# Kernel tuning notes

Measured on AMD Instinct MI355X. Metric: run time of the kernel, lower is better.

## Reference

```python
import jax, jax.numpy as jnp
import numpy as np

HBV_LO = jnp.array([1.0, 50.0, 0.05, 0.01, 0.001, 0.2, 0.0, 0.0, -2.5, 0.5, 0.0, 0.0, 0.3, 0.0], dtype=jnp.float32)
HBV_HI = jnp.array([6.0, 1000.0, 0.9, 0.5, 0.2, 1.0, 10.0, 100.0, 2.5, 10.0, 0.1, 0.2, 5.0, 1.0], dtype=jnp.float32)
TDLST = (1, 13)  # 1-based indices of dynamic parameters (BETA, BETAET)
PRECS = 1e-5


def setup_inputs() -> dict:
    key = jax.random.key(0)
    k1, k2 = jax.random.split(key)
    Nstep, Ngrid, mu = 365, 1000, 16
    x = jax.random.uniform(k1, (Nstep, Ngrid, 3), dtype=jnp.float32)  # [P, T, ETpot]
    parameters = jax.random.uniform(k2, (Nstep, Ngrid, 14, mu), dtype=jnp.float32)
    return {"x": x, "parameters": parameters, "staind": Nstep - 1}


def _hbv_run(x, parameters, staind):
    mu = parameters.shape[-1]
    Nstep, Ngrid, _ = x.shape
    # scale raw [0,1] params to physical ranges: [Nstep, Ngrid, 14, mu]
    parAllTrans = HBV_LO[None, None, :, None] + parameters * (HBV_HI - HBV_LO)[None, None, :, None]
    # dynamic params (tdlst) vary per timestep; others frozen at timestep staind
    dynmask = jnp.zeros((14,), jnp.float32).at[jnp.array([ix - 1 for ix in TDLST])].set(1.0)
    m = dynmask[None, None, :, None]
    parFull = parAllTrans * m + parAllTrans[staind][None] * (1.0 - m)

    s0 = jnp.full((Ngrid, mu), 0.001, dtype=jnp.float32)
    init = (s0, s0, s0, s0, s0)  # SNOWPACK, MELTWATER, SM, SUZ, SLZ

    def step(state, xs):
        SP, MW, SM, SUZ, SLZ = state
        Pv, Tv, Ev, par = xs
        P = Pv[:, None]
        T = Tv[:, None]
        ETp = Ev[:, None]
        BETA, FC, K0, K1, K2, LP, PERCp, UZL, TT, CFMAX, CFR, CWH, BETAET, C = [par[:, i, :] for i in range(14)]
        RAIN = P * (T >= TT).astype(jnp.float32)
        SNOW = P * (T < TT).astype(jnp.float32)
        SP = SP + SNOW
        melt = jnp.minimum(jnp.maximum(CFMAX * (T - TT), 0.0), SP)
        MW = MW + melt
        SP = SP - melt
        refr = jnp.minimum(jnp.maximum(CFR * CFMAX * (TT - T), 0.0), MW)
        SP = SP + refr
        MW = MW - refr
        tosoil = jnp.maximum(MW - CWH * SP, 0.0)
        MW = MW - tosoil
        wet = jnp.clip((SM / FC) ** BETA, 0.0, 1.0)
        recharge = (RAIN + tosoil) * wet
        excess = jnp.maximum(SM - FC, 0.0)
        SM = SM - excess
        evapf = jnp.clip((SM / (LP * FC)) ** BETAET, 0.0, 1.0)
        ETact = jnp.minimum(SM, ETp * evapf)
        SM = jnp.maximum(SM - ETact, PRECS)
        SM = SM + RAIN + tosoil - recharge
        cap = jnp.minimum(SLZ, C * SLZ * (1.0 - jnp.minimum(SM / FC, 1.0)))
        SM = jnp.maximum(SM + cap, PRECS)
        SLZ = jnp.maximum(SLZ - cap, PRECS)
        SUZ = SUZ + recharge + excess
        PERC = jnp.minimum(SUZ, PERCp)
        SUZ = SUZ - PERC
        Q0 = K0 * jnp.maximum(SUZ - UZL, 0.0)
        SUZ = SUZ - Q0
        Q1 = K1 * SUZ
        SUZ = SUZ - Q1
        SLZ = SLZ + PERC
        Q2 = K2 * SLZ
        SLZ = SLZ - Q2
        return (SP, MW, SM, SUZ, SLZ), Q0 + Q1 + Q2

    xs = (x[:, :, 0], x[:, :, 1], x[:, :, 2], parFull)
    _, Qsimmu = jax.lax.scan(step, init, xs)  # [Nstep, Ngrid, mu]
    return Qsimmu.mean(-1)[:, :, None]  # muwts=None, routOpt=False -> [Nstep, Ngrid, 1]


def reference(x, parameters, staind):
    return _hbv_run(x, parameters, staind)
```

## Files before the change

### kernel.cpp

```cpp
#include <hip/hip_runtime.h>


static constexpr int   NSTEP = 365;
static constexpr int   NGRID = 1000;
static constexpr int   MU    = 16;
static constexpr float PRECS = 1e-5f;
static constexpr int   QPAD  = 68;

__global__ __launch_bounds__(64)
__attribute__((amdgpu_waves_per_eu(1, 1)))
void hbv_kernel(const float* __restrict__ x,
                const float* __restrict__ par,
                const int*   __restrict__ staind_p,
                float*       __restrict__ out)
{
    __shared__ float qlds[NSTEP * QPAD];

    const int lane = threadIdx.x;
    const int m    = lane & 15;
    const int gl   = lane >> 4;
    const int gbase = blockIdx.x * 4;
    const int g    = gbase + gl;
    const int staind = *staind_p;

    const size_t tstride = (size_t)NGRID * 14 * MU;
    const int    xstride = NGRID * 3;
    const int    lp = g * (14 * MU) + m;
    const int    lx = g * 3;

    const float* ps = par + (size_t)staind * tstride + lp;
    const float FC    = 50.0f  + ps[ 1*MU] * (1000.0f - 50.0f);
    const float K0    = 0.05f  + ps[ 2*MU] * (0.9f  - 0.05f);
    const float K1    = 0.01f  + ps[ 3*MU] * (0.5f  - 0.01f);
    const float K2    = 0.001f + ps[ 4*MU] * (0.2f  - 0.001f);
    const float LP    = 0.2f   + ps[ 5*MU] * (1.0f  - 0.2f);
    const float PERCp =          ps[ 6*MU] * 10.0f;
    const float UZL   =          ps[ 7*MU] * 100.0f;
    const float TT    = -2.5f  + ps[ 8*MU] * 5.0f;
    const float CFMAX = 0.5f   + ps[ 9*MU] * (10.0f - 0.5f);
    const float CRF   =          ps[10*MU] * 0.1f * CFMAX;
    const float CWH   =          ps[11*MU] * 0.2f;
    const float C     =          ps[13*MU] * 1.0f;
    const float rFC   = 1.0f / FC;
    const float lgFC   = __builtin_amdgcn_logf(FC);
    const float dlg    = lgFC - __builtin_amdgcn_logf(LP * FC);
    const float K1c    = 1.0f - K1;
    const float K2c    = 1.0f - K2;
    const float nK0UZL = -K0 * UZL;

    float SP = 1e-3f, MW = 1e-3f, SM = 1e-3f, SUZ = 1e-3f, SLZ = 1e-3f;

    auto step = [&](float P, float T, float E, float p0, float p12) -> float {
        const float BETA    = fmaf(p0, 5.0f, 1.0f);
        const float BETAET  = fmaf(p12, 4.7f, 0.3f);
        const float dT      = T - TT;
        const float acap    = CFMAX * dT;
        const float bcap    = CRF * (-dT);
        const bool  rc      = (T >= TT);
        const float RAIN    = rc ? P : 0.0f;
        const float SNOW    = rc ? 0.0f : P;
        const float smsuz   = SUZ + SM;

        const float SP1  = SP + SNOW;
        const float melt = __builtin_amdgcn_fmed3f(acap, 0.0f, SP1);
        const float SP2  = SP1 - melt;
        const float MW1  = MW + melt;
        const float refr = __builtin_amdgcn_fmed3f(bcap, 0.0f, MW1);
        const float MW2  = MW1 - refr;
        const float SP3  = SP2 + refr;
        const float lim  = CWH * SP3;
        const float tosoil = fmaxf(MW2 - lim, 0.0f);
        SP = SP3;
        MW = fminf(MW2, lim);

        const float SM1    = fminf(SM, FC);
        const float SUZe   = smsuz - SM1;
        const float lg     = __builtin_amdgcn_logf(SM);
        const float uc     = fminf(lg - lgFC, 0.0f);
        const float wet    = __builtin_amdgcn_exp2f(BETA * uc);
        const float evapf  = __builtin_amdgcn_exp2f(BETAET * fminf(uc + dlg, 0.0f));
        const float SM2    = fmaxf(fmaf(-E, evapf, SM1), PRECS);
        const float rt     = RAIN + tosoil;
        const float recharge = rt * wet;
        const float SM3    = (SM2 + rt) - recharge;
        const float capf   = fmaxf(fmaf(-SM3, rFC, 1.0f), 0.0f);
        const float cap    = (C * SLZ) * capf;
        SM = fmaxf(SM3 + cap, PRECS);
        const float SLZ1   = fmaxf(SLZ - cap, PRECS);

        const float SUZ1 = SUZe + recharge;
        const float PERC = fminf(SUZ1, PERCp);
        const float SUZ2 = fmaxf(SUZ1 - PERCp, 0.0f);
        const float Q0   = fmaxf(fmaf(K0, SUZ2, nK0UZL), 0.0f);
        const float SUZ3 = SUZ2 - Q0;
        const float Q1   = K1 * SUZ3;
        SUZ = K1c * SUZ3;
        const float SLZ2 = SLZ1 + PERC;
        const float Q2   = K2 * SLZ2;
        SLZ = K2c * SLZ2;

        return Q0 + Q1 + Q2;
    };

    float aP[10], aT[10], aE[10], a0[10], a12[10];
    float cP[10], cT[10], cE[10], c0[10], c12[10];
    const float* prow = par;
    const float* xrow = x;

#define LOADB(BP, BT, BE, B0, B12, N)                            \
    _Pragma("unroll") for (int j = 0; j < (N); ++j) {            \
        B0[j]  = prow[lp];                                       \
        B12[j] = prow[lp + 192];                                 \
        const float3 v = *(const float3*)(xrow + lx);            \
        BP[j] = v.x; BT[j] = v.y; BE[j] = v.z;                   \
        prow += tstride; xrow += xstride;                        \
    }

#define COMPB(BP, BT, BE, B0, B12, T0, N)                        \
    {                                                            \
        float qreg[10];                                          \
        _Pragma("unroll") for (int j = 0; j < (N); ++j)          \
            qreg[j] = step(BP[j], BT[j], BE[j], B0[j], B12[j]);  \
        _Pragma("unroll") for (int j = 0; j < (N); ++j)          \
            qlds[((T0) + j) * QPAD + lane] = qreg[j];            \
    }

    LOADB(aP, aT, aE, a0, a12, 10)

    for (int bb = 0; bb < 17; ++bb) {
        const int t0 = bb * 20;
        LOADB(cP, cT, cE, c0, c12, 10)
        COMPB(aP, aT, aE, a0, a12, t0, 10)
        LOADB(aP, aT, aE, a0, a12, 10)
        COMPB(cP, cT, cE, c0, c12, t0 + 10, 10)
    }

    LOADB(cP, cT, cE, c0, c12, 10)
    COMPB(aP, aT, aE, a0, a12, 340, 10)
    LOADB(aP, aT, aE, a0, a12, 5)
    COMPB(cP, cT, cE, c0, c12, 350, 10)
    COMPB(aP, aT, aE, a0, a12, 360, 5)

#undef LOADB
#undef COMPB

    for (int i = lane; i < NSTEP * 4; i += 64) {
        const int t  = i >> 2;
        const int gg = i & 3;
        const float4* row = (const float4*)&qlds[t * QPAD + gg * 16];
        const float4 r0 = row[0], r1 = row[1], r2 = row[2], r3 = row[3];
        const float s0 = (r0.x + r0.y) + (r0.z + r0.w);
        const float s1 = (r1.x + r1.y) + (r1.z + r1.w);
        const float s2 = (r2.x + r2.y) + (r2.z + r2.w);
        const float s3 = (r3.x + r3.y) + (r3.z + r3.w);
        out[t * NGRID + gbase + gg] = ((s0 + s1) + (s2 + s3)) * 0.0625f;
    }
}

extern "C" void kernel_launch(void* const* d_in, const int* in_sizes, int n_in,
                              void* d_out, int out_size, void* d_ws, size_t ws_size,
                              hipStream_t stream) {
    const float* x      = (const float*)d_in[0];
    const float* par    = (const float*)d_in[1];
    const int*   staind = (const int*)d_in[2];
    float*       out    = (float*)d_out;

    hipLaunchKernelGGL(hbv_kernel, dim3(NGRID / 4), dim3(64), 0, stream,
                       x, par, staind, out);
}
```

Before: 53.90 us.

## Process two ensemble members per lane with packed float2 math, halving block count

Each lane now handles two mu members, stored as float2 vectors, so a 64-lane block covers 8 grid cells instead of 4 and only 125 blocks are launched. The aim is to use packed FP32 instructions (v_pk_fma/v_pk_mul/v_pk_add) on MI355X and amortize the per-step scalar P/T/E loads over more work. The cost is that the serial per-lane dependency chain doubles in length and far fewer blocks run concurrently, which reduces parallelism on a chip with many CUs. Transcendental ops and min/max stay scalar.

```diff
diff --git a/kernel.cpp b/kernel.cpp
--- a/kernel.cpp
+++ b/kernel.cpp
@@ -6,6 +6,25 @@
 static constexpr int   MU    = 16;
 static constexpr float PRECS = 1e-5f;
 static constexpr int   QPAD  = 68;
+
+typedef float v2 __attribute__((ext_vector_type(2)));
+
+static __device__ __forceinline__ v2 v2min(v2 a, v2 b) {
+    return (v2){fminf(a.x, b.x), fminf(a.y, b.y)};
+}
+static __device__ __forceinline__ v2 v2max(v2 a, v2 b) {
+    return (v2){fmaxf(a.x, b.x), fmaxf(a.y, b.y)};
+}
+static __device__ __forceinline__ v2 v2med3(v2 a, v2 hi) {
+    return (v2){__builtin_amdgcn_fmed3f(a.x, 0.0f, hi.x),
+                __builtin_amdgcn_fmed3f(a.y, 0.0f, hi.y)};
+}
+static __device__ __forceinline__ v2 v2log(v2 a) {
+    return (v2){__builtin_amdgcn_logf(a.x), __builtin_amdgcn_logf(a.y)};
+}
+static __device__ __forceinline__ v2 v2exp2(v2 a) {
+    return (v2){__builtin_amdgcn_exp2f(a.x), __builtin_amdgcn_exp2f(a.y)};
+}
 
 __global__ __launch_bounds__(64)
 __attribute__((amdgpu_waves_per_eu(1, 1)))
@@ -17,112 +36,117 @@
     __shared__ float qlds[NSTEP * QPAD];
 
     const int lane = threadIdx.x;
-    const int m    = lane & 15;
-    const int gl   = lane >> 4;
-    const int gbase = blockIdx.x * 4;
+    const int ml   = lane & 7;
+    const int gl   = lane >> 3;
+    const int gbase = blockIdx.x * 8;
     const int g    = gbase + gl;
     const int staind = *staind_p;
 
     const size_t tstride = (size_t)NGRID * 14 * MU;
     const int    xstride = NGRID * 3;
-    const int    lp = g * (14 * MU) + m;
+    const int    lp = g * (14 * MU) + ml;
     const int    lx = g * 3;
 
     const float* ps = par + (size_t)staind * tstride + lp;
-    const float FC    = 50.0f  + ps[ 1*MU] * (1000.0f - 50.0f);
-    const float K0    = 0.05f  + ps[ 2*MU] * (0.9f  - 0.05f);
-    const float K1    = 0.01f  + ps[ 3*MU] * (0.5f  - 0.01f);
-    const float K2    = 0.001f + ps[ 4*MU] * (0.2f  - 0.001f);
-    const float LP    = 0.2f   + ps[ 5*MU] * (1.0f  - 0.2f);
-    const float PERCp =          ps[ 6*MU] * 10.0f;
-    const float UZL   =          ps[ 7*MU] * 100.0f;
-    const float TT    = -2.5f  + ps[ 8*MU] * 5.0f;
-    const float CFMAX = 0.5f   + ps[ 9*MU] * (10.0f - 0.5f);
-    const float CRF   =          ps[10*MU] * 0.1f * CFMAX;
-    const float CWH   =          ps[11*MU] * 0.2f;
-    const float C     =          ps[13*MU] * 1.0f;
-    const float rFC   = 1.0f / FC;
-    const float lgFC   = __builtin_amdgcn_logf(FC);
-    const float dlg    = lgFC - __builtin_amdgcn_logf(LP * FC);
-    const float K1c    = 1.0f - K1;
-    const float K2c    = 1.0f - K2;
-    const float nK0UZL = -K0 * UZL;
+#define LD2(i) ((v2){ps[(i)*MU], ps[(i)*MU + 8]})
+    const v2 FC    = 50.0f  + LD2(1) * (1000.0f - 50.0f);
+    const v2 K0    = 0.05f  + LD2(2) * (0.9f  - 0.05f);
+    const v2 K1    = 0.01f  + LD2(3) * (0.5f  - 0.01f);
+    const v2 K2    = 0.001f + LD2(4) * (0.2f  - 0.001f);
+    const v2 LP    = 0.2f   + LD2(5) * (1.0f  - 0.2f);
+    const v2 PERCp =          LD2(6) * 10.0f;
+    const v2 UZL   =          LD2(7) * 100.0f;
+    const v2 TT    = -2.5f  + LD2(8) * 5.0f;
+    const v2 CFMAX = 0.5f   + LD2(9) * (10.0f - 0.5f);
+    const v2 CRF   =          LD2(10) * 0.1f * CFMAX;
+    const v2 CWH   =          LD2(11) * 0.2f;
+    const v2 C     =          LD2(13);
+#undef LD2
+    const v2 rFC    = 1.0f / FC;
+    const v2 lgFC   = v2log(FC);
+    const v2 dlg    = lgFC - v2log(LP * FC);
+    const v2 K1c    = 1.0f - K1;
+    const v2 K2c    = 1.0f - K2;
+    const v2 nK0UZL = -K0 * UZL;
 
-    float SP = 1e-3f, MW = 1e-3f, SM = 1e-3f, SUZ = 1e-3f, SLZ = 1e-3f;
+    v2 SP = 1e-3f, MW = 1e-3f, SM = 1e-3f, SUZ = 1e-3f, SLZ = 1e-3f;
 
-    auto step = [&](float P, float T, float E, float p0, float p12) -> float {
-        const float BETA    = fmaf(p0, 5.0f, 1.0f);
-        const float BETAET  = fmaf(p12, 4.7f, 0.3f);
-        const float dT      = T - TT;
-        const float acap    = CFMAX * dT;
-        const float bcap    = CRF * (-dT);
-        const bool  rc      = (T >= TT);
-        const float RAIN    = rc ? P : 0.0f;
-        const float SNOW    = rc ? 0.0f : P;
-        const float smsuz   = SUZ + SM;
+    auto step = [&](float P, float T, float E, v2 p0, v2 p12) -> float {
+        const v2 BETA   = p0  * 5.0f + 1.0f;
+        const v2 BETAET = p12 * 4.7f + 0.3f;
+        const v2 dT     = T - TT;
+        const v2 acap   = CFMAX * dT;
+        const v2 bcap   = CRF * (-dT);
+        v2 RAIN, SNOW;
+        RAIN.x = (T >= TT.x) ? P : 0.0f;  SNOW.x = (T >= TT.x) ? 0.0f : P;
+        RAIN.y = (T >= TT.y) ? P : 0.0f;  SNOW.y = (T >= TT.y) ? 0.0f : P;
+        const v2 smsuz  = SUZ + SM;
 
-        const float SP1  = SP + SNOW;
-        const float melt = __builtin_amdgcn_fmed3f(acap, 0.0f, SP1);
-        const float SP2  = SP1 - melt;
-        const float MW1  = MW + melt;
-        const float refr = __builtin_amdgcn_fmed3f(bcap, 0.0f, MW1);
-        const float MW2  = MW1 - refr;
-        const float SP3  = SP2 + refr;
-        const float lim  = CWH * SP3;
-        const float tosoil = fmaxf(MW2 - lim, 0.0f);
+        const v2 SP1  = SP + SNOW;
+        const v2 melt = v2med3(acap, SP1);
+        const v2 SP2  = SP1 - melt;
+        const v2 MW1  = MW + melt;
+        const v2 refr = v2med3(bcap, MW1);
+        const v2 MW2  = MW1 - refr;
+        const v2 SP3  = SP2 + refr;
+        const v2 lim  = CWH * SP3;
+        const v2 tosoil = v2max(MW2 - lim, (v2)0.0f);
         SP = SP3;
-        MW = fminf(MW2, lim);
+        MW = v2min(MW2, lim);
 
-        const float SM1    = fminf(SM, FC);
-        const float SUZe   = smsuz - SM1;
-        const float lg     = __builtin_amdgcn_logf(SM);
-        const float uc     = fminf(lg - lgFC, 0.0f);
-        const float wet    = __builtin_amdgcn_exp2f(BETA * uc);
-        const float evapf  = __builtin_amdgcn_exp2f(BETAET * fminf(uc + dlg, 0.0f));
-        const float SM2    = fmaxf(fmaf(-E, evapf, SM1), PRECS);
-        const float rt     = RAIN + tosoil;
-        const float recharge = rt * wet;
-        const float SM3    = (SM2 + rt) - recharge;
-        const float capf   = fmaxf(fmaf(-SM3, rFC, 1.0f), 0.0f);
-        const float cap    = (C * SLZ) * capf;
-        SM = fmaxf(SM3 + cap, PRECS);
-        const float SLZ1   = fmaxf(SLZ - cap, PRECS);
+        const v2 SM1   = v2min(SM, FC);
+        const v2 SUZe  = smsuz - SM1;
+        const v2 lg    = v2log(SM);
+        const v2 uc    = v2min(lg - lgFC, (v2)0.0f);
+        const v2 wet   = v2exp2(BETA * uc);
+        const v2 evapf = v2exp2(BETAET * v2min(uc + dlg, (v2)0.0f));
+        const v2 SM2   = v2max(SM1 - E * evapf, (v2)PRECS);
+        const v2 rt    = RAIN + tosoil;
+        const v2 recharge = rt * wet;
+        const v2 SM3   = (SM2 + rt) - recharge;
+        const v2 capf  = v2max(1.0f - SM3 * rFC, (v2)0.0f);
+        const v2 cap   = (C * SLZ) * capf;
+        SM = v2max(SM3 + cap, (v2)PRECS);
+        const v2 SLZ1  = v2max(SLZ - cap, (v2)PRECS);
 
-        const float SUZ1 = SUZe + recharge;
-        const float PERC = fminf(SUZ1, PERCp);
-        const float SUZ2 = fmaxf(SUZ1 - PERCp, 0.0f);
-        const float Q0   = fmaxf(fmaf(K0, SUZ2, nK0UZL), 0.0f);
-        const float SUZ3 = SUZ2 - Q0;
-        const float Q1   = K1 * SUZ3;
+        const v2 SUZ1 = SUZe + recharge;
+        const v2 PERC = v2min(SUZ1, PERCp);
+        const v2 SUZ2 = v2max(SUZ1 - PERCp, (v2)0.0f);
+        const v2 Q0   = v2max(K0 * SUZ2 + nK0UZL, (v2)0.0f);
+        const v2 SUZ3 = SUZ2 - Q0;
+        const v2 Q1   = K1 * SUZ3;
         SUZ = K1c * SUZ3;
-        const float SLZ2 = SLZ1 + PERC;
-        const float Q2   = K2 * SLZ2;
+        const v2 SLZ2 = SLZ1 + PERC;
+        const v2 Q2   = K2 * SLZ2;
         SLZ = K2c * SLZ2;
 
-        return Q0 + Q1 + Q2;
+        const v2 q = Q0 + Q1 + Q2;
+        return q.x + q.y;
     };
 
-    float aP[10], aT[10], aE[10], a0[10], a12[10];
-    float cP[10], cT[10], cE[10], c0[10], c12[10];
+    float aP[10], aT[10], aE[10];
+    v2    a0[10], a12[10];
+    float cP[10], cT[10], cE[10];
+    v2    c0[10], c12[10];
     const float* prow = par;
     const float* xrow = x;
 
-#define LOADB(BP, BT, BE, B0, B12, N)                            \
-    _Pragma("unroll") for (int j = 0; j < (N); ++j) {            \
-        B0[j]  = prow[lp];                                       \
-        B12[j] = prow[lp + 192];                                 \
-        const float3 v = *(const float3*)(xrow + lx);            \
-        BP[j] = v.x; BT[j] = v.y; BE[j] = v.z;                   \
-        prow += tstride; xrow += xstride;                        \
+#define LOADB(BP, BT, BE, B0, B12, N)                                 \
+    _Pragma("unroll") for (int j = 0; j < (N); ++j) {                 \
+        B0[j]  = (v2){prow[lp],       prow[lp + 8]};                  \
+        B12[j] = (v2){prow[lp + 192], prow[lp + 200]};                \
+        const float3 v = *(const float3*)(xrow + lx);                 \
+        BP[j] = v.x; BT[j] = v.y; BE[j] = v.z;                        \
+        prow += tstride; xrow += xstride;                             \
     }
 
-#define COMPB(BP, BT, BE, B0, B12, T0, N)                        \
-    {                                                            \
-        float qreg[10];                                          \
-        _Pragma("unroll") for (int j = 0; j < (N); ++j)          \
-            qreg[j] = step(BP[j], BT[j], BE[j], B0[j], B12[j]);  \
-        _Pragma("unroll") for (int j = 0; j < (N); ++j)          \
-            qlds[((T0) + j) * QPAD + lane] = qreg[j];            \
+#define COMPB(BP, BT, BE, B0, B12, T0, N)                             \
+    {                                                                 \
+        float qreg[10];                                               \
+        _Pragma("unroll") for (int j = 0; j < (N); ++j)               \
+            qreg[j] = step(BP[j], BT[j], BE[j], B0[j], B12[j]);       \
+        _Pragma("unroll") for (int j = 0; j < (N); ++j)               \
+            qlds[((T0) + j) * QPAD + lane] = qreg[j];                 \
     }
 
     LOADB(aP, aT, aE, a0, a12, 10)
@@ -144,16 +168,14 @@
 #undef LOADB
 #undef COMPB
 
-    for (int i = lane; i < NSTEP * 4; i += 64) {
-        const int t  = i >> 2;
-        const int gg = i & 3;
-        const float4* row = (const float4*)&qlds[t * QPAD + gg * 16];
-        const float4 r0 = row[0], r1 = row[1], r2 = row[2], r3 = row[3];
+    for (int i = lane; i < NSTEP * 8; i += 64) {
+        const int t  = i >> 3;
+        const int gg = i & 7;
+        const float4* row = (const float4*)&qlds[t * QPAD + gg * 8];
+        const float4 r0 = row[0], r1 = row[1];
         const float s0 = (r0.x + r0.y) + (r0.z + r0.w);
         const float s1 = (r1.x + r1.y) + (r1.z + r1.w);
-        const float s2 = (r2.x + r2.y) + (r2.z + r2.w);
-        const float s3 = (r3.x + r3.y) + (r3.z + r3.w);
-        out[t * NGRID + gbase + gg] = ((s0 + s1) + (s2 + s3)) * 0.0625f;
+        out[t * NGRID + gbase + gg] = (s0 + s1) * 0.0625f;
     }
 }
 
@@ -165,6 +187,6 @@
     const int*   staind = (const int*)d_in[2];
     float*       out    = (float*)d_out;
 
-    hipLaunchKernelGGL(hbv_kernel, dim3(NGRID / 4), dim3(64), 0, stream,
+    hipLaunchKernelGGL(hbv_kernel, dim3(NGRID / 8), dim3(64), 0, stream,
                        x, par, staind, out);
 }
```

Result: slower. 74.62 us (+38.4%).
